# Performance work log

Hardware: AMD Instinct MI355X
Metric: run time of the kernel (lower is better)

Reference implementation:

```python
import jax, jax.numpy as jnp
import numpy as np

EPS = 1e-5  # BatchNorm eps (torch default)
K = 16      # num_neighbors


def _bn(x, gamma, beta, axes):
    # training-mode BatchNorm (biased variance), channel axis = 1
    mu = x.mean(axes, keepdims=True)
    var = x.var(axes, keepdims=True)
    shp = [1] * x.ndim
    shp[1] = -1
    return (x - mu) * jax.lax.rsqrt(var + EPS) * gamma.reshape(shp) + beta.reshape(shp)


def setup_inputs() -> dict:
    key = jax.random.key(0)
    ks = jax.random.split(key, 6)
    B, C, N, E = 4, 3, 4096, 256
    s = lambda k_, shp, fan: jax.random.normal(k_, shp, jnp.float32) * np.float32(1.0 / np.sqrt(fan))
    return {
        "x": jax.random.normal(ks[0], (B, C, N), jnp.float32),
        "g1": jnp.ones((C,), jnp.float32), "b1": jnp.zeros((C,), jnp.float32),
        "W1": s(ks[1], (E, C), C), "bw1": jnp.zeros((E,), jnp.float32),
        "g2a": jnp.ones((C,), jnp.float32), "b2a": jnp.zeros((C,), jnp.float32),
        "W2a": s(ks[2], (E, C), C),
        "g2b": jnp.ones((E,), jnp.float32), "b2b": jnp.zeros((E,), jnp.float32),
        "W2b": s(ks[3], (E, E), E),
        "Wf": s(ks[4], (E, 2 * E), 2 * E), "bf": jnp.zeros((E,), jnp.float32),
    }


def reference(x, g1, b1, W1, bw1, g2a, b2a, W2a, g2b, b2b, W2b, Wf, bf):
    B, C, N = x.shape
    xn = _bn(x, g1, b1, (0, 2))                               # BatchNorm1d
    point_emb = jnp.einsum('ec,bcn->ben', W1, xn) + bw1[None, :, None]  # conv1 (1x1)
    # dist = -||xi - xj||; torch topk(dist, largest=False) picks the K LARGEST
    # distances. Squared distance is monotone in the norm, so top_k on d2 gives
    # identical indices without materializing [B,3,N,N].
    x2 = jnp.sum(xn * xn, axis=1)                             # [B,N]
    d2 = x2[:, :, None] + x2[:, None, :] - 2.0 * jnp.einsum('bcn,bcm->bnm', xn, xn)
    _, idx = jax.lax.top_k(d2, min(K, N))                     # [B,N,K]
    idx = idx[:, :, 1:]                                       # original loop skips index 0
    gathered = jax.vmap(lambda xb, ib: xb[:, ib])(xn, idx)    # [B,C,N,K-1]
    neigh = gathered - xn[:, :, :, None]                      # edge features
    h = _bn(neigh, g2a, b2a, (0, 2, 3))                       # BatchNorm2d(Cin)
    h = jnp.einsum('ec,bcnk->benk', W2a, h)                   # 1x1 conv, no bias
    h = jax.nn.gelu(_bn(h, g2b, b2b, (0, 2, 3)), approximate=False)
    h = jnp.einsum('fe,benk->bfnk', W2b, h)                   # 1x1 conv, no bias
    neigh_emb = h.max(-1)                                     # max over neighbors
    feat = jnp.concatenate([point_emb, neigh_emb], axis=1)    # [B,2E,N]
    return jnp.einsum('of,bfn->bon', Wf, feat) + bf[None, :, None]
```

## Files before the change

### kernel.cpp

```cpp
#include <hip/hip_runtime.h>
#include <float.h>
#include <math.h>

#define EPS 1e-5f
constexpr int B = 4, C = 3, N = 4096, E = 256;
constexpr int KNN = 15;
constexpr int BN_ = B * N;
constexpr int P = 4;
constexpr int SR  = 264;
constexpr int SRF = 520;

typedef short bf8 __attribute__((ext_vector_type(8)));
typedef float f4  __attribute__((ext_vector_type(4)));

static __device__ __forceinline__ unsigned short f2bf(float f) {
    union { float f; unsigned int u; } v; v.f = f;
    unsigned int r = v.u + 0x7FFFu + ((v.u >> 16) & 1u);
    return (unsigned short)(r >> 16);
}
static __device__ __forceinline__ bf8 ld_bf8(const unsigned short* p) {
    return *(const bf8*)p;
}
static __device__ __forceinline__ float gelu_f(float v) {
    float u = fabsf(v) * 0.70710678118654752f;
    float tt = __builtin_amdgcn_rcpf(1.f + 0.3275911f * u);
    float poly = tt * (0.254829592f + tt * (-0.284496736f + tt * (1.421413741f
               + tt * (-1.453152027f + tt * 1.061405429f))));
    float erfu = 1.f - poly * __expf(-u * u);
    float cdf = 0.5f + 0.5f * (v < 0.f ? -erfu : erfu);
    return v * cdf;
}

__global__ void bn1_stats(const float* __restrict__ x, float* __restrict__ bn1) {
    int c = blockIdx.x, t = threadIdx.x;
    float s = 0.f, ss = 0.f;
    for (int i4 = t; i4 < BN_ / 4; i4 += 256) {
        int b = i4 >> 10, n4 = i4 & 1023;
        float4 v = ((const float4*)(x + (b * C + c) * N))[n4];
        s += v.x + v.y + v.z + v.w;
        ss += v.x * v.x + v.y * v.y + v.z * v.z + v.w * v.w;
    }
    __shared__ float rs_[256], rss_[256];
    rs_[t] = s; rss_[t] = ss; __syncthreads();
    for (int w = 128; w > 0; w >>= 1) {
        if (t < w) { rs_[t] += rs_[t + w]; rss_[t] += rss_[t + w]; }
        __syncthreads();
    }
    if (t == 0) {
        float mu = rs_[0] / (float)BN_;
        float var = rss_[0] / (float)BN_ - mu * mu;
        bn1[c] = mu; bn1[3 + c] = rsqrtf(var + EPS);
    }
}

__global__ void compute_xn_cvt(const float* __restrict__ x,
                               const float* __restrict__ g1,
                               const float* __restrict__ b1,
                               const float* __restrict__ bn1,
                               float4* __restrict__ xn4,
                               const float* __restrict__ W2b, const float* __restrict__ Wf,
                               unsigned short* __restrict__ w2b_t, unsigned short* __restrict__ wf_t) {
    int blk = blockIdx.x;
    if (blk < BN_ / 256) {
        int i = blk * 256 + threadIdx.x;
        int b = i >> 12, n = i & (N - 1);
        float v[3];
        #pragma unroll
        for (int c = 0; c < C; c++)
            v[c] = (x[(b * C + c) * N + n] - bn1[c]) * bn1[3 + c] * g1[c] + b1[c];
        float4 o; o.x = v[0]; o.y = v[1]; o.z = v[2];
        o.w = v[0] * v[0] + v[1] * v[1] + v[2] * v[2];
        xn4[i] = o;
        return;
    }
    int ch = (blk - BN_ / 256) * 256 + threadIdx.x;
    if (ch < 8192) {
        int lane = ch & 63, kb = (ch >> 6) & 7, ft16 = ch >> 9;
        int row = ft16 * 16 + (lane & 15);
        int col = kb * 32 + (lane >> 4) * 8;
        #pragma unroll
        for (int j = 0; j < 8; j++)
            w2b_t[ch * 8 + j] = f2bf(W2b[row * 256 + col + j]);
    } else {
        int c2 = ch - 8192;
        int lane = c2 & 63, kb = (c2 >> 6) & 15, ot = c2 >> 10;
        int row = ot * 16 + (lane & 15);
        int col = kb * 32 + (lane >> 4) * 8;
        #pragma unroll
        for (int j = 0; j < 8; j++)
            wf_t[c2 * 8 + j] = f2bf(Wf[row * 512 + col + j]);
    }
}

__global__ void __launch_bounds__(256, 4) knn_kernel(const float4* __restrict__ xn4,
                                                     unsigned short* __restrict__ idxout,
                                                     float* __restrict__ S9) {
    __shared__ float smom[4][15][9];
    int w = threadIdx.x >> 6, lane = threadIdx.x & 63;
    int i = blockIdx.x * 4 + w;
    int b = i >> 12, n = i & (N - 1);
    const float4* xb = xn4 + b * N;
    float4 qv = xb[n];
    float d[64];
    #pragma unroll
    for (int s = 0; s < 64; s++) {
        float4 p = xb[s * 64 + lane];
        d[s] = qv.w + p.w - 2.f * (qv.x * p.x + qv.y * p.y + qv.z * p.z);
    }
    float cm[8];
    #pragma unroll
    for (int c = 0; c < 8; c++) {
        float v = d[c * 8];
        #pragma unroll
        for (int s = 1; s < 8; s++) v = fmaxf(v, d[c * 8 + s]);
        cm[c] = v;
    }
    float bv = cm[0];
    #pragma unroll
    for (int c = 1; c < 8; c++) bv = fmaxf(bv, cm[c]);

    int myj = 0;
    for (int r = 0; r < 16; r++) {
        float wv = bv;
        #pragma unroll
        for (int off = 32; off > 0; off >>= 1)
            wv = fmaxf(wv, __shfl_xor(wv, off));
        unsigned long long msk = __ballot(bv == wv);
        int wl = __ffsll(msk) - 1;
        int gi = 0;
        if (lane == wl) {
            int cstar = 0; bool got = false;
            #pragma unroll
            for (int c = 0; c < 8; c++) {
                bool h = !got && (cm[c] == bv);
                cstar = h ? c : cstar;
                got = got || h;
            }
            int slot = 0;
            #pragma unroll
            for (int c = 0; c < 8; c++) {
                if (c == cstar) {
                    bool g2 = false;
                    #pragma unroll
                    for (int s = 0; s < 8; s++) {
                        bool h = !g2 && (d[c * 8 + s] == bv);
                        slot = h ? (c * 8 + s) : slot;
                        g2 = g2 || h;
                    }
                    #pragma unroll
                    for (int s = 0; s < 8; s++)
                        d[c * 8 + s] = (c * 8 + s == slot) ? -FLT_MAX : d[c * 8 + s];
                    float v = d[c * 8];
                    #pragma unroll
                    for (int s = 1; s < 8; s++) v = fmaxf(v, d[c * 8 + s]);
                    cm[c] = v;
                }
            }
            bv = cm[0];
            #pragma unroll
            for (int c = 1; c < 8; c++) bv = fmaxf(bv, cm[c]);
            gi = slot * 64 + lane;
        }
        int g = __shfl(gi, wl);
        if (lane == r - 1) myj = g;
    }

    bool act = lane < 15;
    if (act) idxout[i * KNN + lane] = (unsigned short)myj;
    float4 pj = xb[act ? myj : n];
    float v0 = pj.x - qv.x, v1 = pj.y - qv.y, v2 = pj.z - qv.z;
    if (act) {
        float* mm = smom[w][lane];
        mm[0] = v0; mm[1] = v1; mm[2] = v2;
        mm[3] = v0 * v0; mm[4] = v1 * v1; mm[5] = v2 * v2;
        mm[6] = v0 * v1; mm[7] = v0 * v2; mm[8] = v1 * v2;
    }
    __syncthreads();
    int t = threadIdx.x;
    if (t < 36) {
        int wsel = t / 9, j = t % 9;
        float a = 0.f;
        #pragma unroll
        for (int u = 0; u < 15; u++) a += smom[wsel][u][j];
        atomicAdd(&S9[((blockIdx.x * 4 + wsel) & 63) * 9 + j], a);
    }
}

__global__ void finalize_stats(const float* __restrict__ S9,
                               const float* __restrict__ g2a, const float* __restrict__ b2a,
                               const float* __restrict__ W2a,
                               const float* __restrict__ g2b, const float* __restrict__ b2b,
                               float* __restrict__ ab, float* __restrict__ sc, float* __restrict__ sh) {
    const float cnt = (float)(BN_ * KNN);
    __shared__ float S[9];
    __shared__ float alpha[3], beta[3], mu[3], Ehh[3][3];
    int t = threadIdx.x;
    if (t < 9) {
        float a = 0.f;
        for (int u = 0; u < 64; u++) a += S9[u * 9 + t];
        S[t] = a;
    }
    __syncthreads();
    if (t == 0) {
        float m[3];
        float s2[3][3];
        s2[0][0] = S[3]; s2[1][1] = S[4]; s2[2][2] = S[5];
        s2[0][1] = s2[1][0] = S[6]; s2[0][2] = s2[2][0] = S[7]; s2[1][2] = s2[2][1] = S[8];
        for (int c = 0; c < 3; c++) {
            m[c] = S[c] / cnt;
            float var = s2[c][c] / cnt - m[c] * m[c];
            alpha[c] = g2a[c] * rsqrtf(var + EPS);
            beta[c]  = b2a[c] - m[c] * alpha[c];
            mu[c] = m[c];
            ab[c] = alpha[c]; ab[3 + c] = beta[c];
        }
        for (int c = 0; c < 3; c++)
            for (int cc = 0; cc < 3; cc++)
                Ehh[c][cc] = alpha[c] * alpha[cc] * (s2[c][cc] / cnt)
                           + alpha[c] * beta[cc] * m[c]
                           + beta[c] * alpha[cc] * m[cc]
                           + beta[c] * beta[cc];
    }
    __syncthreads();
    int e = t;
    float wv[3], Eh[3];
    for (int c = 0; c < 3; c++) { wv[c] = W2a[e * 3 + c]; Eh[c] = alpha[c] * mu[c] + beta[c]; }
    float mean = wv[0] * Eh[0] + wv[1] * Eh[1] + wv[2] * Eh[2];
    float m2 = 0.f;
    for (int c = 0; c < 3; c++)
        for (int cc = 0; cc < 3; cc++) m2 += wv[c] * wv[cc] * Ehh[c][cc];
    float var = m2 - mean * mean;
    float s = g2b[e] * rsqrtf(var + EPS);
    sc[e] = s;
    sh[e] = b2b[e] - mean * s;
}

__global__ void __launch_bounds__(256, 4) fused_final(
        const float4* __restrict__ xn4, const unsigned short* __restrict__ idx,
        const float* __restrict__ ab,
        const float* __restrict__ W2a,
        const float* __restrict__ sc, const float* __restrict__ sh,
        const unsigned short* __restrict__ w2b_t,
        const float* __restrict__ W1, const float* __restrict__ bw1,
        const unsigned short* __restrict__ wf_t, const float* __restrict__ bfv,
        float* __restrict__ out) {
    __shared__ __align__(16) unsigned short hh_bf[64 * SR];
    __shared__ __align__(16) unsigned short feat_bf[4 * SRF];
    __shared__ float hhat[P][3][16];
    int i0 = blockIdx.x * P;
    int t = threadIdx.x;
    int b = i0 >> 12, n0 = i0 & (N - 1);
    const float4* xb = xn4 + b * N;

    if (t < P * KNN) {
        int p = t / KNN, k = t % KNN;
        int j = idx[(i0 + p) * KNN + k];
        float4 pj = xb[j];
        float4 pn = xb[n0 + p];
        hhat[p][0][k] = ab[0] * (pj.x - pn.x) + ab[3];
        hhat[p][1][k] = ab[1] * (pj.y - pn.y) + ab[4];
        hhat[p][2][k] = ab[2] * (pj.z - pn.z) + ab[5];
    }
    __syncthreads();

    {
        int e = t;
        float w0 = W2a[e * 3], w1 = W2a[e * 3 + 1], w2 = W2a[e * 3 + 2];
        float s = sc[e], o = sh[e];
        #pragma unroll
        for (int p = 0; p < P; p++) {
            float g0 = 0.f;
            #pragma unroll
            for (int k = 0; k < KNN; k++) {
                float v = s * (w0 * hhat[p][0][k] + w1 * hhat[p][1][k] + w2 * hhat[p][2][k]) + o;
                float g = gelu_f(v);
                hh_bf[(16 * p + k) * SR + e] = f2bf(g);
                if (k == 0) g0 = g;
            }
            hh_bf[(16 * p + 15) * SR + e] = f2bf(g0);
            float4 pv = xb[n0 + p];
            feat_bf[p * SRF + e] = f2bf(bw1[e] + W1[e * 3] * pv.x
                       + W1[e * 3 + 1] * pv.y + W1[e * 3 + 2] * pv.z);
        }
    }
    __syncthreads();

    int w = t >> 6, lane = t & 63;
    int m = lane & 15, q = lane >> 4;

    {
        int fh = w >> 1, pp = w & 1;
        bf8 hfr[2][8];
        #pragma unroll
        for (int pi = 0; pi < 2; pi++)
            #pragma unroll
            for (int kb = 0; kb < 8; kb++)
                hfr[pi][kb] = ld_bf8(&hh_bf[(16 * (pp * 2 + pi) + m) * SR + kb * 32 + q * 8]);

        const unsigned short* wbase = w2b_t + fh * 8 * 4096 + lane * 8;
        for (int ft = 0; ft < 8; ft++) {
            bf8 a[8];
            #pragma unroll
            for (int kb = 0; kb < 8; kb++)
                a[kb] = ld_bf8(wbase + ft * 4096 + kb * 512);
            #pragma unroll
            for (int pi = 0; pi < 2; pi++) {
                f4 acc = {0.f, 0.f, 0.f, 0.f};
                #pragma unroll
                for (int kb = 0; kb < 8; kb++)
                    acc = __builtin_amdgcn_mfma_f32_16x16x32_bf16(hfr[pi][kb], a[kb], acc, 0, 0, 0);
                float mx = fmaxf(fmaxf(acc[0], acc[1]), fmaxf(acc[2], acc[3]));
                mx = fmaxf(mx, __shfl_xor(mx, 16));
                mx = fmaxf(mx, __shfl_xor(mx, 32));
                if (lane < 16)
                    feat_bf[(pp * 2 + pi) * SRF + E + (fh * 8 + ft) * 16 + lane] = f2bf(mx);
            }
        }
    }
    __syncthreads();

    {
        bf8 fb[16];
        #pragma unroll
        for (int kb = 0; kb < 16; kb++)
            fb[kb] = ld_bf8(&feat_bf[(m & 3) * SRF + kb * 32 + q * 8]);
        const unsigned short* wfb = wf_t + w * 4 * 8192 + lane * 8;
        #pragma unroll
        for (int ot = 0; ot < 4; ot++) {
            f4 acc = {0.f, 0.f, 0.f, 0.f};
            #pragma unroll
            for (int kb = 0; kb < 16; kb++) {
                bf8 a = ld_bf8(wfb + ot * 8192 + kb * 512);
                acc = __builtin_amdgcn_mfma_f32_16x16x32_bf16(a, fb[kb], acc, 0, 0, 0);
            }
            if (m < P) {
                int o0 = (w * 4 + ot) * 16 + 4 * q;
                out[(b * E + o0 + 0) * N + n0 + m] = acc[0] + bfv[o0 + 0];
                out[(b * E + o0 + 1) * N + n0 + m] = acc[1] + bfv[o0 + 1];
                out[(b * E + o0 + 2) * N + n0 + m] = acc[2] + bfv[o0 + 2];
                out[(b * E + o0 + 3) * N + n0 + m] = acc[3] + bfv[o0 + 3];
            }
        }
    }
}

extern "C" void kernel_launch(void* const* d_in, const int* in_sizes, int n_in,
                              void* d_out, int out_size, void* d_ws, size_t ws_size,
                              hipStream_t stream) {
    (void)in_sizes; (void)n_in; (void)out_size; (void)ws_size;
    const float* x   = (const float*)d_in[0];
    const float* g1  = (const float*)d_in[1];
    const float* b1  = (const float*)d_in[2];
    const float* W1  = (const float*)d_in[3];
    const float* bw1 = (const float*)d_in[4];
    const float* g2a = (const float*)d_in[5];
    const float* b2a = (const float*)d_in[6];
    const float* W2a = (const float*)d_in[7];
    const float* g2b = (const float*)d_in[8];
    const float* b2b = (const float*)d_in[9];
    const float* W2b = (const float*)d_in[10];
    const float* Wf  = (const float*)d_in[11];
    const float* bfv = (const float*)d_in[12];
    float* out = (float*)d_out;

    char* ws = (char*)d_ws;
    size_t off = 0;
    auto alloc = [&](size_t bytes) { size_t o = off; off = (off + bytes + 255) & ~(size_t)255; return o; };
    float4* xn4           = (float4*)(ws + alloc(sizeof(float4) * BN_));
    unsigned short* idx   = (unsigned short*)(ws + alloc(sizeof(unsigned short) * BN_ * KNN));
    float* bn1            = (float*)(ws + alloc(sizeof(float) * 8));
    float* S9             = (float*)(ws + alloc(sizeof(float) * 64 * 9));
    float* ab             = (float*)(ws + alloc(sizeof(float) * 8));
    float* sc             = (float*)(ws + alloc(sizeof(float) * E));
    float* sh             = (float*)(ws + alloc(sizeof(float) * E));
    unsigned short* w2bt  = (unsigned short*)(ws + alloc(sizeof(unsigned short) * E * E));
    unsigned short* wft   = (unsigned short*)(ws + alloc(sizeof(unsigned short) * E * 2 * E));

    hipMemsetAsync(S9, 0, sizeof(float) * 64 * 9, stream);

    bn1_stats<<<C, 256, 0, stream>>>(x, bn1);
    compute_xn_cvt<<<BN_ / 256 + (8192 + 16384) / 256, 256, 0, stream>>>(
        x, g1, b1, bn1, xn4, W2b, Wf, w2bt, wft);
    knn_kernel<<<BN_ / 4, 256, 0, stream>>>(xn4, idx, S9);
    finalize_stats<<<1, 256, 0, stream>>>(S9, g2a, b2a, W2a, g2b, b2b, ab, sc, sh);
    fused_final<<<BN_ / P, 256, 0, stream>>>(xn4, idx, ab, W2a, sc, sh, w2bt, W1, bw1, wft, bfv, out);
}
```

Measured before the change: 271.7 us.

## Use tanh-form GELU, prefold BN scale into conv weights, restripe W2b MFMA loop

Replaces the erf-polynomial GELU with a tanh/sigmoid approximation computed from one exp and one reciprocal. Folds the BN2b scale and shift into the W2a weights in finalize_stats, so each edge needs only three FMAs, and stores hhat as float4 for vector LDS reads. Restructures the W2b MFMA stage so each wave owns 4 output tiles across all 4 points. The weight fragments are loaded once per tile and the h fragments are re-read from LDS instead of being held in registers. The tanh GELU differs slightly from exact erf GELU, which is within bf16 tolerance but is an approximation.

Measured after the change: 388.7 us. 1.43x slower.

```diff
diff --git a/kernel.cpp b/kernel.cpp
--- a/kernel.cpp
+++ b/kernel.cpp
@@ -21,14 +21,10 @@
 static __device__ __forceinline__ bf8 ld_bf8(const unsigned short* p) {
     return *(const bf8*)p;
 }
-static __device__ __forceinline__ float gelu_f(float v) {
-    float u = fabsf(v) * 0.70710678118654752f;
-    float tt = __builtin_amdgcn_rcpf(1.f + 0.3275911f * u);
-    float poly = tt * (0.254829592f + tt * (-0.284496736f + tt * (1.421413741f
-               + tt * (-1.453152027f + tt * 1.061405429f))));
-    float erfu = 1.f - poly * __expf(-u * u);
-    float cdf = 0.5f + 0.5f * (v < 0.f ? -erfu : erfu);
-    return v * cdf;
+static __device__ __forceinline__ float gelu_t(float v) {
+    float z = v * fmaf(v * v, 0.07135482f, 1.59576912f);
+    float r = __builtin_amdgcn_rcpf(1.f + __expf(z));
+    return fmaf(-v, r, v);
 }
 
 __global__ void bn1_stats(const float* __restrict__ x, float* __restrict__ bn1) {
@@ -190,7 +186,7 @@
                                const float* __restrict__ g2a, const float* __restrict__ b2a,
                                const float* __restrict__ W2a,
                                const float* __restrict__ g2b, const float* __restrict__ b2b,
-                               float* __restrict__ ab, float* __restrict__ sc, float* __restrict__ sh) {
+                               float* __restrict__ ab, float4* __restrict__ wsb) {
     const float cnt = (float)(BN_ * KNN);
     __shared__ float S[9];
     __shared__ float alpha[3], beta[3], mu[3], Ehh[3][3];
@@ -231,22 +227,22 @@
         for (int cc = 0; cc < 3; cc++) m2 += wv[c] * wv[cc] * Ehh[c][cc];
     float var = m2 - mean * mean;
     float s = g2b[e] * rsqrtf(var + EPS);
-    sc[e] = s;
-    sh[e] = b2b[e] - mean * s;
+    float4 o;
+    o.x = wv[0] * s; o.y = wv[1] * s; o.z = wv[2] * s; o.w = b2b[e] - mean * s;
+    wsb[e] = o;
 }
 
 __global__ void __launch_bounds__(256, 4) fused_final(
         const float4* __restrict__ xn4, const unsigned short* __restrict__ idx,
         const float* __restrict__ ab,
-        const float* __restrict__ W2a,
-        const float* __restrict__ sc, const float* __restrict__ sh,
+        const float4* __restrict__ wsb,
         const unsigned short* __restrict__ w2b_t,
         const float* __restrict__ W1, const float* __restrict__ bw1,
         const unsigned short* __restrict__ wf_t, const float* __restrict__ bfv,
         float* __restrict__ out) {
     __shared__ __align__(16) unsigned short hh_bf[64 * SR];
     __shared__ __align__(16) unsigned short feat_bf[4 * SRF];
-    __shared__ float hhat[P][3][16];
+    __shared__ __align__(16) float4 hhat4[P][16];
     int i0 = blockIdx.x * P;
     int t = threadIdx.x;
     int b = i0 >> 12, n0 = i0 & (N - 1);
@@ -257,23 +253,26 @@
         int j = idx[(i0 + p) * KNN + k];
         float4 pj = xb[j];
         float4 pn = xb[n0 + p];
-        hhat[p][0][k] = ab[0] * (pj.x - pn.x) + ab[3];
-        hhat[p][1][k] = ab[1] * (pj.y - pn.y) + ab[4];
-        hhat[p][2][k] = ab[2] * (pj.z - pn.z) + ab[5];
+        float4 h;
+        h.x = ab[0] * (pj.x - pn.x) + ab[3];
+        h.y = ab[1] * (pj.y - pn.y) + ab[4];
+        h.z = ab[2] * (pj.z - pn.z) + ab[5];
+        h.w = 0.f;
+        hhat4[p][k] = h;
     }
     __syncthreads();
 
     {
         int e = t;
-        float w0 = W2a[e * 3], w1 = W2a[e * 3 + 1], w2 = W2a[e * 3 + 2];
-        float s = sc[e], o = sh[e];
+        float4 w4 = wsb[e];
         #pragma unroll
         for (int p = 0; p < P; p++) {
             float g0 = 0.f;
             #pragma unroll
             for (int k = 0; k < KNN; k++) {
-                float v = s * (w0 * hhat[p][0][k] + w1 * hhat[p][1][k] + w2 * hhat[p][2][k]) + o;
-                float g = gelu_f(v);
+                float4 hv = hhat4[p][k];
+                float v = fmaf(w4.x, hv.x, fmaf(w4.y, hv.y, fmaf(w4.z, hv.z, w4.w)));
+                float g = gelu_t(v);
                 hh_bf[(16 * p + k) * SR + e] = f2bf(g);
                 if (k == 0) g0 = g;
             }
@@ -289,31 +288,25 @@
     int m = lane & 15, q = lane >> 4;
 
     {
-        int fh = w >> 1, pp = w & 1;
-        bf8 hfr[2][8];
-        #pragma unroll
-        for (int pi = 0; pi < 2; pi++)
+        for (int ftl = 0; ftl < 4; ftl++) {
+            int ftg = w * 4 + ftl;
+            bf8 a[8];
             #pragma unroll
             for (int kb = 0; kb < 8; kb++)
-                hfr[pi][kb] = ld_bf8(&hh_bf[(16 * (pp * 2 + pi) + m) * SR + kb * 32 + q * 8]);
-
-        const unsigned short* wbase = w2b_t + fh * 8 * 4096 + lane * 8;
-        for (int ft = 0; ft < 8; ft++) {
-            bf8 a[8];
-            #pragma unroll
-            for (int kb = 0; kb < 8; kb++)
-                a[kb] = ld_bf8(wbase + ft * 4096 + kb * 512);
-            #pragma unroll
-            for (int pi = 0; pi < 2; pi++) {
+                a[kb] = ld_bf8(w2b_t + ftg * 4096 + kb * 512 + lane * 8);
+            #pragma unroll
+            for (int pi = 0; pi < 4; pi++) {
                 f4 acc = {0.f, 0.f, 0.f, 0.f};
                 #pragma unroll
-                for (int kb = 0; kb < 8; kb++)
-                    acc = __builtin_amdgcn_mfma_f32_16x16x32_bf16(hfr[pi][kb], a[kb], acc, 0, 0, 0);
+                for (int kb = 0; kb < 8; kb++) {
+                    bf8 h = ld_bf8(&hh_bf[(16 * pi + m) * SR + kb * 32 + q * 8]);
+                    acc = __builtin_amdgcn_mfma_f32_16x16x32_bf16(h, a[kb], acc, 0, 0, 0);
+                }
                 float mx = fmaxf(fmaxf(acc[0], acc[1]), fmaxf(acc[2], acc[3]));
                 mx = fmaxf(mx, __shfl_xor(mx, 16));
                 mx = fmaxf(mx, __shfl_xor(mx, 32));
                 if (lane < 16)
-                    feat_bf[(pp * 2 + pi) * SRF + E + (fh * 8 + ft) * 16 + lane] = f2bf(mx);
+                    feat_bf[pi * SRF + E + ftg * 16 + lane] = f2bf(mx);
             }
         }
     }
@@ -371,8 +364,7 @@
     float* bn1            = (float*)(ws + alloc(sizeof(float) * 8));
     float* S9             = (float*)(ws + alloc(sizeof(float) * 64 * 9));
     float* ab             = (float*)(ws + alloc(sizeof(float) * 8));
-    float* sc             = (float*)(ws + alloc(sizeof(float) * E));
-    float* sh             = (float*)(ws + alloc(sizeof(float) * E));
+    float4* wsb           = (float4*)(ws + alloc(sizeof(float4) * E));
     unsigned short* w2bt  = (unsigned short*)(ws + alloc(sizeof(unsigned short) * E * E));
     unsigned short* wft   = (unsigned short*)(ws + alloc(sizeof(unsigned short) * E * 2 * E));
 
@@ -382,6 +374,6 @@
     compute_xn_cvt<<<BN_ / 256 + (8192 + 16384) / 256, 256, 0, stream>>>(
         x, g1, b1, bn1, xn4, W2b, Wf, w2bt, wft);
     knn_kernel<<<BN_ / 4, 256, 0, stream>>>(xn4, idx, S9);
-    finalize_stats<<<1, 256, 0, stream>>>(S9, g2a, b2a, W2a, g2b, b2b, ab, sc, sh);
-    fused_final<<<BN_ / P, 256, 0, stream>>>(xn4, idx, ab, W2a, sc, sh, w2bt, W1, bw1, wft, bfv, out);
-}
+    finalize_stats<<<1, 256, 0, stream>>>(S9, g2a, b2a, W2a, g2b, b2b, ab, wsb);
+    fused_final<<<BN_ / P, 256, 0, stream>>>(xn4, idx, ab, wsb, w2bt, W1, bw1, wft, bfv, out);
+}
```
